# Optimization experiments

Measured on AMD Instinct MI355X. Metric: run time of the kernel, lower is better.

Reference implementation:

```python
import jax, jax.numpy as jnp
import numpy as np

T, B, D, H, L, O = 800, 32, 440, 1024, 4, 2000
EPS = 1e-5

def _bn(x, g, b, m, v):
    return (x - m) * jax.lax.rsqrt(v + EPS) * g + b

def setup_inputs() -> dict:
    key = jax.random.key(0)
    ks = jax.random.split(key, 12)
    s = 0.02
    return {
        "xs": jax.random.normal(ks[0], (T, B, D), dtype=jnp.float32),
        "w0": jax.random.normal(ks[1], (2 * H, D), dtype=jnp.float32) * s,
        "wr": jax.random.normal(ks[2], (L - 1, 2 * H, H), dtype=jnp.float32) * s,
        "bnz_g": jnp.ones((L, H), jnp.float32),
        "bnz_b": jnp.zeros((L, H), jnp.float32),
        "bnz_m": jax.random.normal(ks[3], (L, H), dtype=jnp.float32) * 0.1,
        "bnz_v": jax.random.uniform(ks[4], (L, H), dtype=jnp.float32) + 0.5,
        "bnc_g": jnp.ones((L, H), jnp.float32),
        "bnc_b": jnp.zeros((L, H), jnp.float32),
        "bnc_m": jax.random.normal(ks[5], (L, H), dtype=jnp.float32) * 0.1,
        "bnc_v": jax.random.uniform(ks[6], (L, H), dtype=jnp.float32) + 0.5,
        "wf": jax.random.normal(ks[7], (O, H), dtype=jnp.float32) * 0.003,
        "bnf_g": jnp.ones((O,), jnp.float32),
        "bnf_b": jnp.zeros((O,), jnp.float32),
        "bnf_m": jax.random.normal(ks[8], (O,), dtype=jnp.float32) * 0.1,
        "bnf_v": jax.random.uniform(ks[9], (O,), dtype=jnp.float32) + 0.5,
    }

def reference(xs, w0, wr, bnz_g, bnz_b, bnz_m, bnz_v, bnc_g, bnc_b, bnc_m, bnc_v, wf, bnf_g, bnf_b, bnf_m, bnf_v):
    x = xs  # [T,B,feat]
    for i in range(L):
        W = w0 if i == 0 else wr[i - 1]
        ws = jnp.einsum('tbd,hd->tbh', x, W)          # [T,B,2H]
        wz, wc = jnp.split(ws, 2, axis=-1)
        z = jax.nn.sigmoid(_bn(wz, bnz_g[i], bnz_b[i], bnz_m[i], bnz_v[i]))
        c = jax.nn.relu(_bn(wc, bnc_g[i], bnc_b[i], bnc_m[i], bnc_v[i]))
        def step(h, zc):
            z_t, c_t = zc
            h = (1.0 - z_t) * c_t + z_t * h
            return h, h
        _, hs = jax.lax.scan(step, jnp.zeros((B, H), x.dtype), (z, c))
        x = hs  # [T,B,H]
    out = jnp.einsum('tbh,oh->tbo', x, wf).reshape(T * B, O)
    out = _bn(out, bnf_g, bnf_b, bnf_m, bnf_v)
    return jax.nn.log_softmax(out, axis=1)
```

## Files before the change

### kernel.cpp

```cpp
#include <hip/hip_runtime.h>
#include <math.h>
#include <stdint.h>

#define T_ 800
#define B_ 32
#define D_ 440
#define DP_ 448
#define H_ 1024
#define L_ 4
#define O_ 2000
#define OP_ 2048
#define EPS_ 1e-5f
#define M_ (T_ * B_)
#define NC_ 8
#define TC_ (T_ / NC_)

#define BM 128
#define BN 128
#define BK 32

typedef __attribute__((ext_vector_type(8))) short bf16x8;
typedef __attribute__((ext_vector_type(4))) float f32x4;

__device__ inline float b2f(unsigned short u) {
    union { unsigned int i; float f; } v; v.i = ((unsigned int)u) << 16; return v.f;
}
__device__ inline unsigned short f2b(float f) {
    unsigned int x = __float_as_uint(f);
    return (unsigned short)((x + 0x7FFFu + ((x >> 16) & 1u)) >> 16);
}

__global__ void bn_prep(const float* __restrict__ g, const float* __restrict__ b,
                        const float* __restrict__ m, const float* __restrict__ v,
                        float* __restrict__ scale, float* __restrict__ bias,
                        int nsrc, int ndst)
{
    int i = blockIdx.x * 256 + threadIdx.x;
    if (i >= ndst) return;
    if (i < nsrc) {
        float s = g[i] * rsqrtf(v[i] + EPS_);
        scale[i] = s;
        bias[i] = fmaf(-m[i], s, b[i]);
    } else {
        scale[i] = 0.f;
        bias[i] = 0.f;
    }
}

__global__ void cvt_pad(const float* __restrict__ src, unsigned short* __restrict__ dst,
                        int Rs, int Cs, int Cd, int total)
{
    int i = blockIdx.x * 256 + threadIdx.x;
    if (i >= total) return;
    int r = i / Cd, c = i - r * Cd;
    float v = (r < Rs && c < Cs) ? src[(size_t)r * Cs + c] : 0.f;
    dst[i] = f2b(v);
}

__global__ __launch_bounds__(256) void gemm_bf16(
    const unsigned short* __restrict__ A, const unsigned short* __restrict__ Wt,
    int K, int mode,
    unsigned short* __restrict__ zout, unsigned short* __restrict__ cout,
    const float* __restrict__ zscale, const float* __restrict__ zbias,
    const float* __restrict__ cscale, const float* __restrict__ cbias,
    unsigned short* __restrict__ fout,
    const float* __restrict__ fscale, const float* __restrict__ fbias)
{
    __shared__ unsigned short As[BM * BK];
    __shared__ unsigned short Bs[BN * BK];

    const int tid = threadIdx.x;
    const int lane = tid & 63;
    const int wid = tid >> 6;
    const int wm = wid >> 1, wn = wid & 1;
    const int m0 = blockIdx.y * BM;
    const int n0 = blockIdx.x * BN;

    const int srow = lane >> 2;
    const int scol = (lane & 3) * 8;

    const int ca0 = wid * 2, ca1 = wid * 2 + 1;
    const unsigned short* aR0 = A + (size_t)(m0 + ca0 * 16 + srow) * K + scol;
    const unsigned short* aR1 = A + (size_t)(m0 + ca1 * 16 + srow) * K + scol;
    const int gn0 = n0 + ((ca0 >> 2) << 6) + srow * 4 + (ca0 & 3);
    const int gn1 = n0 + ((ca1 >> 2) << 6) + srow * 4 + (ca1 & 3);
    const unsigned short* bR0 = Wt + (size_t)gn0 * K + scol;
    const unsigned short* bR1 = Wt + (size_t)gn1 * K + scol;
    unsigned short* lA0 = As + ca0 * 16 * BK;
    unsigned short* lA1 = As + ca1 * 16 * BK;
    unsigned short* lB0 = Bs + ca0 * 16 * BK;
    unsigned short* lB1 = Bs + ca1 * 16 * BK;

    f32x4 acc[4][4];
    #pragma unroll
    for (int i = 0; i < 4; i++)
        #pragma unroll
        for (int j = 0; j < 4; j++)
            acc[i][j] = (f32x4){0.f, 0.f, 0.f, 0.f};

    const int fr = lane & 15;
    const int fk = (lane >> 4) * 8;

    for (int k0 = 0; k0 < K; k0 += BK) {
        __builtin_amdgcn_global_load_lds(
            (const __attribute__((address_space(1))) unsigned int*)(aR0 + k0),
            (__attribute__((address_space(3))) unsigned int*)lA0, 16, 0, 0);
        __builtin_amdgcn_global_load_lds(
            (const __attribute__((address_space(1))) unsigned int*)(aR1 + k0),
            (__attribute__((address_space(3))) unsigned int*)lA1, 16, 0, 0);
        __builtin_amdgcn_global_load_lds(
            (const __attribute__((address_space(1))) unsigned int*)(bR0 + k0),
            (__attribute__((address_space(3))) unsigned int*)lB0, 16, 0, 0);
        __builtin_amdgcn_global_load_lds(
            (const __attribute__((address_space(1))) unsigned int*)(bR1 + k0),
            (__attribute__((address_space(3))) unsigned int*)lB1, 16, 0, 0);
        __syncthreads();

        bf16x8 af[4], bfr[4];
        #pragma unroll
        for (int t = 0; t < 4; t++) {
            af[t]  = *(const bf16x8*)(As + (wm * 64 + t * 16 + fr) * BK + fk);
            bfr[t] = *(const bf16x8*)(Bs + (wn * 64 + t * 16 + fr) * BK + fk);
        }
        #pragma unroll
        for (int mi = 0; mi < 4; mi++)
            #pragma unroll
            for (int ni = 0; ni < 4; ni++)
                acc[mi][ni] = __builtin_amdgcn_mfma_f32_16x16x32_bf16(af[mi], bfr[ni], acc[mi][ni], 0, 0, 0);
        __syncthreads();
    }

    const int q = lane >> 4;
    const int colb = n0 + wn * 64 + (lane & 15) * 4;
    const int rbase = m0 + wm * 64 + q * 4;

    if (mode == 0) {
        const bool isz = (n0 < H_);
        const float* sc = isz ? zscale : cscale;
        const float* bi = isz ? zbias : cbias;
        unsigned short* dst = isz ? zout : cout;
        const int npb = isz ? colb : colb - H_;
        const float4 s4 = *(const float4*)(sc + npb);
        const float4 b4 = *(const float4*)(bi + npb);
        #pragma unroll
        for (int mi = 0; mi < 4; mi++)
            #pragma unroll
            for (int r = 0; r < 4; r++) {
                const int m = rbase + mi * 16 + r;
                float v0 = fmaf(acc[mi][0][r], s4.x, b4.x);
                float v1 = fmaf(acc[mi][1][r], s4.y, b4.y);
                float v2 = fmaf(acc[mi][2][r], s4.z, b4.z);
                float v3 = fmaf(acc[mi][3][r], s4.w, b4.w);
                if (isz) {
                    v0 = __builtin_amdgcn_rcpf(1.f + __expf(-v0));
                    v1 = __builtin_amdgcn_rcpf(1.f + __expf(-v1));
                    v2 = __builtin_amdgcn_rcpf(1.f + __expf(-v2));
                    v3 = __builtin_amdgcn_rcpf(1.f + __expf(-v3));
                } else {
                    v0 = fmaxf(v0, 0.f); v1 = fmaxf(v1, 0.f);
                    v2 = fmaxf(v2, 0.f); v3 = fmaxf(v3, 0.f);
                }
                ushort4 pk = make_ushort4(f2b(v0), f2b(v1), f2b(v2), f2b(v3));
                *(ushort4*)(dst + (size_t)m * H_ + npb) = pk;
            }
    } else {
        const float4 s4 = *(const float4*)(fscale + colb);
        const float4 b4 = *(const float4*)(fbias + colb);
        #pragma unroll
        for (int mi = 0; mi < 4; mi++)
            #pragma unroll
            for (int r = 0; r < 4; r++) {
                const int m = rbase + mi * 16 + r;
                ushort4 pk = make_ushort4(
                    f2b(fmaf(acc[mi][0][r], s4.x, b4.x)),
                    f2b(fmaf(acc[mi][1][r], s4.y, b4.y)),
                    f2b(fmaf(acc[mi][2][r], s4.z, b4.z)),
                    f2b(fmaf(acc[mi][3][r], s4.w, b4.w)));
                *(ushort4*)(fout + (size_t)m * OP_ + colb) = pk;
            }
    }
}

__global__ __launch_bounds__(256) void scan_pass1(
    const unsigned short* __restrict__ z, const unsigned short* __restrict__ c,
    float* __restrict__ H0, float* __restrict__ P)
{
    const int k = blockIdx.y;
    const int idx = blockIdx.x * 256 + threadIdx.x;
    float h = 0.f, p = 1.f;
    size_t off = (size_t)k * TC_ * (B_ * H_) + idx;
    #pragma unroll 4
    for (int t = 0; t < TC_; ++t) {
        float zt = b2f(z[off]);
        float ct = b2f(c[off]);
        h = fmaf(zt, h - ct, ct);
        p *= zt;
        off += (size_t)(B_ * H_);
    }
    H0[(size_t)k * (B_ * H_) + idx] = h;
    P[(size_t)k * (B_ * H_) + idx] = p;
}

__global__ __launch_bounds__(256) void scan_pass2(
    const unsigned short* __restrict__ z, const unsigned short* __restrict__ c,
    const float* __restrict__ H0, const float* __restrict__ P,
    unsigned short* __restrict__ x)
{
    const int k = blockIdx.y;
    const int idx = blockIdx.x * 256 + threadIdx.x;
    float h = 0.f;
    for (int j = 0; j < k; ++j)
        h = fmaf(P[(size_t)j * (B_ * H_) + idx], h, H0[(size_t)j * (B_ * H_) + idx]);
    size_t off = (size_t)k * TC_ * (B_ * H_) + idx;
    #pragma unroll 4
    for (int t = 0; t < TC_; ++t) {
        float zt = b2f(z[off]);
        float ct = b2f(c[off]);
        h = fmaf(zt, h - ct, ct);
        x[off] = f2b(h);
        off += (size_t)(B_ * H_);
    }
}

__global__ __launch_bounds__(256) void logsoftmax_kernel(
    const unsigned short* __restrict__ lg, float* __restrict__ out)
{
    const int row = blockIdx.x;
    const unsigned short* p = lg + (size_t)row * OP_;
    float* po = out + (size_t)row * O_;
    const int tid = threadIdx.x;

    float v[8];
    float mx = -1e30f;
    #pragma unroll
    for (int j = 0; j < 8; j++) {
        int col = tid + j * 256;
        v[j] = (col < O_) ? b2f(p[col]) : -1e30f;
        mx = fmaxf(mx, v[j]);
    }
    #pragma unroll
    for (int o = 32; o > 0; o >>= 1) mx = fmaxf(mx, __shfl_down(mx, o));
    __shared__ float smax[4];
    __shared__ float ssum[4];
    const int lane = tid & 63, wid = tid >> 6;
    if (lane == 0) smax[wid] = mx;
    __syncthreads();
    mx = fmaxf(fmaxf(smax[0], smax[1]), fmaxf(smax[2], smax[3]));

    float s = 0.f;
    #pragma unroll
    for (int j = 0; j < 8; j++) {
        int col = tid + j * 256;
        if (col < O_) s += expf(v[j] - mx);
    }
    #pragma unroll
    for (int o = 32; o > 0; o >>= 1) s += __shfl_down(s, o);
    if (lane == 0) ssum[wid] = s;
    __syncthreads();
    s = ssum[0] + ssum[1] + ssum[2] + ssum[3];
    const float lse = mx + logf(s);

    #pragma unroll
    for (int j = 0; j < 8; j++) {
        int col = tid + j * 256;
        if (col < O_) po[col] = v[j] - lse;
    }
}

extern "C" void kernel_launch(void* const* d_in, const int* in_sizes, int n_in,
                              void* d_out, int out_size, void* d_ws, size_t ws_size,
                              hipStream_t stream)
{
    (void)in_sizes; (void)n_in; (void)out_size; (void)ws_size;

    const float* xs    = (const float*)d_in[0];
    const float* w0    = (const float*)d_in[1];
    const float* wr    = (const float*)d_in[2];
    const float* bnz_g = (const float*)d_in[3];
    const float* bnz_b = (const float*)d_in[4];
    const float* bnz_m = (const float*)d_in[5];
    const float* bnz_v = (const float*)d_in[6];
    const float* bnc_g = (const float*)d_in[7];
    const float* bnc_b = (const float*)d_in[8];
    const float* bnc_m = (const float*)d_in[9];
    const float* bnc_v = (const float*)d_in[10];
    const float* wf    = (const float*)d_in[11];
    const float* bnf_g = (const float*)d_in[12];
    const float* bnf_b = (const float*)d_in[13];
    const float* bnf_m = (const float*)d_in[14];
    const float* bnf_v = (const float*)d_in[15];
    float* out = (float*)d_out;

    unsigned short* p = (unsigned short*)d_ws;
    unsigned short* xbuf  = p;  p += (size_t)M_ * H_;
    unsigned short* x0buf = p;  p += (size_t)M_ * DP_;
    unsigned short* zbuf  = p;  p += (size_t)M_ * H_;
    unsigned short* cbuf  = p;  p += (size_t)M_ * H_;
    unsigned short* w0p   = p;  p += (size_t)(2 * H_) * DP_;
    unsigned short* wrp   = p;  p += (size_t)(L_ - 1) * (2 * H_) * H_;
    unsigned short* wfp   = p;  p += (size_t)OP_ * H_;
    unsigned short* lbuf  = p;  p += (size_t)M_ * OP_;
    float* fp = (float*)p;
    float* zs = fp;  fp += L_ * H_;
    float* zb = fp;  fp += L_ * H_;
    float* cs = fp;  fp += L_ * H_;
    float* cb = fp;  fp += L_ * H_;
    float* fs = fp;  fp += OP_;
    float* fb = fp;  fp += OP_;
    float* sH0 = fp; fp += NC_ * B_ * H_;
    float* sP  = fp;

    dim3 blk(256);
    bn_prep<<<(L_ * H_ + 255) / 256, blk, 0, stream>>>(bnz_g, bnz_b, bnz_m, bnz_v, zs, zb, L_ * H_, L_ * H_);
    bn_prep<<<(L_ * H_ + 255) / 256, blk, 0, stream>>>(bnc_g, bnc_b, bnc_m, bnc_v, cs, cb, L_ * H_, L_ * H_);
    bn_prep<<<(OP_ + 255) / 256, blk, 0, stream>>>(bnf_g, bnf_b, bnf_m, bnf_v, fs, fb, O_, OP_);

    {
        int t0 = M_ * DP_;
        cvt_pad<<<(t0 + 255) / 256, blk, 0, stream>>>(xs, x0buf, M_, D_, DP_, t0);
        int t1 = 2 * H_ * DP_;
        cvt_pad<<<(t1 + 255) / 256, blk, 0, stream>>>(w0, w0p, 2 * H_, D_, DP_, t1);
        int t2 = (L_ - 1) * 2 * H_ * H_;
        cvt_pad<<<(t2 + 255) / 256, blk, 0, stream>>>(wr, wrp, (L_ - 1) * 2 * H_, H_, H_, t2);
        int t3 = OP_ * H_;
        cvt_pad<<<(t3 + 255) / 256, blk, 0, stream>>>(wf, wfp, O_, H_, H_, t3);
    }

    dim3 sgrid((B_ * H_) / 256, NC_);
    for (int layer = 0; layer < L_; ++layer) {
        const unsigned short* Ain = (layer == 0) ? x0buf : xbuf;
        const unsigned short* W   = (layer == 0) ? w0p : (wrp + (size_t)(layer - 1) * (2 * H_) * H_);
        const int K               = (layer == 0) ? DP_ : H_;
        dim3 grid((2 * H_) / BN, M_ / BM);
        gemm_bf16<<<grid, blk, 0, stream>>>(Ain, W, K, 0,
            zbuf, cbuf,
            zs + layer * H_, zb + layer * H_, cs + layer * H_, cb + layer * H_,
            nullptr, nullptr, nullptr);
        scan_pass1<<<sgrid, blk, 0, stream>>>(zbuf, cbuf, sH0, sP);
        scan_pass2<<<sgrid, blk, 0, stream>>>(zbuf, cbuf, sH0, sP, xbuf);
    }

    dim3 gridf(OP_ / BN, M_ / BM);
    gemm_bf16<<<gridf, blk, 0, stream>>>(xbuf, wfp, H_, 1,
        nullptr, nullptr, nullptr, nullptr, nullptr, nullptr,
        lbuf, fs, fb);

    logsoftmax_kernel<<<M_, blk, 0, stream>>>(lbuf, out);
}
```

Baseline: 1.328 ms.

## Double-buffer GEMM LDS tiles, vectorize scan and conversion kernels, more scan chunks

```diff
diff --git a/kernel.cpp b/kernel.cpp
--- a/kernel.cpp
+++ b/kernel.cpp
@@ -12,7 +12,8 @@
 #define OP_ 2048
 #define EPS_ 1e-5f
 #define M_ (T_ * B_)
-#define NC_ 8
+#define BH_ (B_ * H_)
+#define NC_ 16
 #define TC_ (T_ / NC_)
 
 #define BM 128
@@ -47,14 +48,26 @@
     }
 }
 
-__global__ void cvt_pad(const float* __restrict__ src, unsigned short* __restrict__ dst,
-                        int Rs, int Cs, int Cd, int total)
+__global__ void cvt_pad8(const float* __restrict__ src, unsigned short* __restrict__ dst,
+                         int Rs, int Cs, int Cd, int total8)
 {
     int i = blockIdx.x * 256 + threadIdx.x;
-    if (i >= total) return;
-    int r = i / Cd, c = i - r * Cd;
-    float v = (r < Rs && c < Cs) ? src[(size_t)r * Cs + c] : 0.f;
-    dst[i] = f2b(v);
+    if (i >= total8) return;
+    const int c8 = Cd >> 3;
+    int r = i / c8, c = (i - r * c8) << 3;
+    ushort4 lo, hi;
+    if (r < Rs && c < Cs) {
+        const float4 a = *(const float4*)(src + (size_t)r * Cs + c);
+        const float4 b = *(const float4*)(src + (size_t)r * Cs + c + 4);
+        lo = make_ushort4(f2b(a.x), f2b(a.y), f2b(a.z), f2b(a.w));
+        hi = make_ushort4(f2b(b.x), f2b(b.y), f2b(b.z), f2b(b.w));
+    } else {
+        lo = make_ushort4(0, 0, 0, 0);
+        hi = make_ushort4(0, 0, 0, 0);
+    }
+    unsigned short* d = dst + (size_t)r * Cd + c;
+    *(ushort4*)d = lo;
+    *(ushort4*)(d + 4) = hi;
 }
 
 __global__ __launch_bounds__(256) void gemm_bf16(
@@ -66,8 +79,8 @@
     unsigned short* __restrict__ fout,
     const float* __restrict__ fscale, const float* __restrict__ fbias)
 {
-    __shared__ unsigned short As[BM * BK];
-    __shared__ unsigned short Bs[BN * BK];
+    __shared__ unsigned short As[2][BM * BK];
+    __shared__ unsigned short Bs[2][BN * BK];
 
     const int tid = threadIdx.x;
     const int lane = tid & 63;
@@ -86,10 +99,8 @@
     const int gn1 = n0 + ((ca1 >> 2) << 6) + srow * 4 + (ca1 & 3);
     const unsigned short* bR0 = Wt + (size_t)gn0 * K + scol;
     const unsigned short* bR1 = Wt + (size_t)gn1 * K + scol;
-    unsigned short* lA0 = As + ca0 * 16 * BK;
-    unsigned short* lA1 = As + ca1 * 16 * BK;
-    unsigned short* lB0 = Bs + ca0 * 16 * BK;
-    unsigned short* lB1 = Bs + ca1 * 16 * BK;
+    const int lofsA0 = ca0 * 16 * BK;
+    const int lofsA1 = ca1 * 16 * BK;
 
     f32x4 acc[4][4];
     #pragma unroll
@@ -101,33 +112,56 @@
     const int fr = lane & 15;
     const int fk = (lane >> 4) * 8;
 
-    for (int k0 = 0; k0 < K; k0 += BK) {
+    const int nIters = K / BK;
+
+    {
         __builtin_amdgcn_global_load_lds(
-            (const __attribute__((address_space(1))) unsigned int*)(aR0 + k0),
-            (__attribute__((address_space(3))) unsigned int*)lA0, 16, 0, 0);
+            (const __attribute__((address_space(1))) unsigned int*)aR0,
+            (__attribute__((address_space(3))) unsigned int*)(As[0] + lofsA0), 16, 0, 0);
         __builtin_amdgcn_global_load_lds(
-            (const __attribute__((address_space(1))) unsigned int*)(aR1 + k0),
-            (__attribute__((address_space(3))) unsigned int*)lA1, 16, 0, 0);
+            (const __attribute__((address_space(1))) unsigned int*)aR1,
+            (__attribute__((address_space(3))) unsigned int*)(As[0] + lofsA1), 16, 0, 0);
         __builtin_amdgcn_global_load_lds(
-            (const __attribute__((address_space(1))) unsigned int*)(bR0 + k0),
-            (__attribute__((address_space(3))) unsigned int*)lB0, 16, 0, 0);
+            (const __attribute__((address_space(1))) unsigned int*)bR0,
+            (__attribute__((address_space(3))) unsigned int*)(Bs[0] + lofsA0), 16, 0, 0);
         __builtin_amdgcn_global_load_lds(
-            (const __attribute__((address_space(1))) unsigned int*)(bR1 + k0),
-            (__attribute__((address_space(3))) unsigned int*)lB1, 16, 0, 0);
+            (const __attribute__((address_space(1))) unsigned int*)bR1,
+            (__attribute__((address_space(3))) unsigned int*)(Bs[0] + lofsA1), 16, 0, 0);
+    }
+
+    for (int it = 0; it < nIters; ++it) {
         __syncthreads();
 
+        if (it + 1 < nIters) {
+            const int nk = (it + 1) * BK;
+            const int nb = (it + 1) & 1;
+            __builtin_amdgcn_global_load_lds(
+                (const __attribute__((address_space(1))) unsigned int*)(aR0 + nk),
+                (__attribute__((address_space(3))) unsigned int*)(As[nb] + lofsA0), 16, 0, 0);
+            __builtin_amdgcn_global_load_lds(
+                (const __attribute__((address_space(1))) unsigned int*)(aR1 + nk),
+                (__attribute__((address_space(3))) unsigned int*)(As[nb] + lofsA1), 16, 0, 0);
+            __builtin_amdgcn_global_load_lds(
+                (const __attribute__((address_space(1))) unsigned int*)(bR0 + nk),
+                (__attribute__((address_space(3))) unsigned int*)(Bs[nb] + lofsA0), 16, 0, 0);
+            __builtin_amdgcn_global_load_lds(
+                (const __attribute__((address_space(1))) unsigned int*)(bR1 + nk),
+                (__attribute__((address_space(3))) unsigned int*)(Bs[nb] + lofsA1), 16, 0, 0);
+        }
+
+        const unsigned short* curA = As[it & 1];
+        const unsigned short* curB = Bs[it & 1];
         bf16x8 af[4], bfr[4];
         #pragma unroll
         for (int t = 0; t < 4; t++) {
-            af[t]  = *(const bf16x8*)(As + (wm * 64 + t * 16 + fr) * BK + fk);
-            bfr[t] = *(const bf16x8*)(Bs + (wn * 64 + t * 16 + fr) * BK + fk);
+            af[t]  = *(const bf16x8*)(curA + (wm * 64 + t * 16 + fr) * BK + fk);
+            bfr[t] = *(const bf16x8*)(curB + (wn * 64 + t * 16 + fr) * BK + fk);
         }
         #pragma unroll
         for (int mi = 0; mi < 4; mi++)
             #pragma unroll
             for (int ni = 0; ni < 4; ni++)
                 acc[mi][ni] = __builtin_amdgcn_mfma_f32_16x16x32_bf16(af[mi], bfr[ni], acc[mi][ni], 0, 0, 0);
-        __syncthreads();
     }
 
     const int q = lane >> 4;
@@ -186,19 +220,22 @@
     float* __restrict__ H0, float* __restrict__ P)
 {
     const int k = blockIdx.y;
-    const int idx = blockIdx.x * 256 + threadIdx.x;
-    float h = 0.f, p = 1.f;
-    size_t off = (size_t)k * TC_ * (B_ * H_) + idx;
-    #pragma unroll 4
+    const int e2 = blockIdx.x * 256 + threadIdx.x;
+    float h0 = 0.f, h1 = 0.f, p0 = 1.f, p1 = 1.f;
+    size_t off = ((size_t)k * TC_ * BH_ + 2 * e2) >> 1;
+    const unsigned int* z32 = (const unsigned int*)z;
+    const unsigned int* c32 = (const unsigned int*)c;
+    #pragma unroll 5
     for (int t = 0; t < TC_; ++t) {
-        float zt = b2f(z[off]);
-        float ct = b2f(c[off]);
-        h = fmaf(zt, h - ct, ct);
-        p *= zt;
-        off += (size_t)(B_ * H_);
-    }
-    H0[(size_t)k * (B_ * H_) + idx] = h;
-    P[(size_t)k * (B_ * H_) + idx] = p;
+        unsigned int zz = z32[off], cc = c32[off];
+        float z0 = b2f((unsigned short)zz), z1 = b2f((unsigned short)(zz >> 16));
+        float c0 = b2f((unsigned short)cc), c1 = b2f((unsigned short)(cc >> 16));
+        h0 = fmaf(z0, h0 - c0, c0);  p0 *= z0;
+        h1 = fmaf(z1, h1 - c1, c1);  p1 *= z1;
+        off += BH_ / 2;
+    }
+    *(float2*)(H0 + (size_t)k * BH_ + 2 * e2) = make_float2(h0, h1);
+    *(float2*)(P  + (size_t)k * BH_ + 2 * e2) = make_float2(p0, p1);
 }
 
 __global__ __launch_bounds__(256) void scan_pass2(
@@ -207,18 +244,27 @@
     unsigned short* __restrict__ x)
 {
     const int k = blockIdx.y;
-    const int idx = blockIdx.x * 256 + threadIdx.x;
-    float h = 0.f;
-    for (int j = 0; j < k; ++j)
-        h = fmaf(P[(size_t)j * (B_ * H_) + idx], h, H0[(size_t)j * (B_ * H_) + idx]);
-    size_t off = (size_t)k * TC_ * (B_ * H_) + idx;
-    #pragma unroll 4
+    const int e2 = blockIdx.x * 256 + threadIdx.x;
+    float h0 = 0.f, h1 = 0.f;
+    for (int j = 0; j < k; ++j) {
+        float2 pj = *(const float2*)(P  + (size_t)j * BH_ + 2 * e2);
+        float2 hj = *(const float2*)(H0 + (size_t)j * BH_ + 2 * e2);
+        h0 = fmaf(pj.x, h0, hj.x);
+        h1 = fmaf(pj.y, h1, hj.y);
+    }
+    size_t off = ((size_t)k * TC_ * BH_ + 2 * e2) >> 1;
+    const unsigned int* z32 = (const unsigned int*)z;
+    const unsigned int* c32 = (const unsigned int*)c;
+    unsigned int* x32 = (unsigned int*)x;
+    #pragma unroll 5
     for (int t = 0; t < TC_; ++t) {
-        float zt = b2f(z[off]);
-        float ct = b2f(c[off]);
-        h = fmaf(zt, h - ct, ct);
-        x[off] = f2b(h);
-        off += (size_t)(B_ * H_);
+        unsigned int zz = z32[off], cc = c32[off];
+        float z0 = b2f((unsigned short)zz), z1 = b2f((unsigned short)(zz >> 16));
+        float c0 = b2f((unsigned short)cc), c1 = b2f((unsigned short)(cc >> 16));
+        h0 = fmaf(z0, h0 - c0, c0);
+        h1 = fmaf(z1, h1 - c1, c1);
+        x32[off] = (unsigned int)f2b(h0) | ((unsigned int)f2b(h1) << 16);
+        off += BH_ / 2;
     }
 }
 
@@ -307,7 +353,7 @@
     float* cb = fp;  fp += L_ * H_;
     float* fs = fp;  fp += OP_;
     float* fb = fp;  fp += OP_;
-    float* sH0 = fp; fp += NC_ * B_ * H_;
+    float* sH0 = fp; fp += NC_ * BH_;
     float* sP  = fp;
 
     dim3 blk(256);
@@ -316,17 +362,18 @@
     bn_prep<<<(OP_ + 255) / 256, blk, 0, stream>>>(bnf_g, bnf_b, bnf_m, bnf_v, fs, fb, O_, OP_);
 
     {
-        int t0 = M_ * DP_;
-        cvt_pad<<<(t0 + 255) / 256, blk, 0, stream>>>(xs, x0buf, M_, D_, DP_, t0);
-        int t1 = 2 * H_ * DP_;
-        cvt_pad<<<(t1 + 255) / 256, blk, 0, stream>>>(w0, w0p, 2 * H_, D_, DP_, t1);
-        int t2 = (L_ - 1) * 2 * H_ * H_;
-        cvt_pad<<<(t2 + 255) / 256, blk, 0, stream>>>(wr, wrp, (L_ - 1) * 2 * H_, H_, H_, t2);
-        int t3 = OP_ * H_;
-        cvt_pad<<<(t3 + 255) / 256, blk, 0, stream>>>(wf, wfp, O_, H_, H_, t3);
-    }
-
-    dim3 sgrid((B_ * H_) / 256, NC_);
+        int t0 = M_ * DP_ / 8;
+        cvt_pad8<<<(t0 + 255) / 256, blk, 0, stream>>>(xs, x0buf, M_, D_, DP_, t0);
+        int t1 = 2 * H_ * DP_ / 8;
+        cvt_pad8<<<(t1 + 255) / 256, blk, 0, stream>>>(w0, w0p, 2 * H_, D_, DP_, t1);
+        int t2 = (L_ - 1) * 2 * H_ * H_ / 8;
+        cvt_pad8<<<(t2 + 255) / 256, blk, 0, stream>>>(wr, wrp, (L_ - 1) * 2 * H_, H_, H_, t2);
+        int t3 = OP_ * H_ / 8;
+        cvt_pad8<<<(t3 + 255) / 256, blk, 0, stream>>>(wf, wfp, O_, H_, H_, t3);
+    }
+
+    dim3 sgrid1(BH_ / 512, NC_ - 1);
+    dim3 sgrid2(BH_ / 512, NC_);
     for (int layer = 0; layer < L_; ++layer) {
         const unsigned short* Ain = (layer == 0) ? x0buf : xbuf;
         const unsigned short* W   = (layer == 0) ? w0p : (wrp + (size_t)(layer - 1) * (2 * H_) * H_);
@@ -336,8 +383,8 @@
             zbuf, cbuf,
             zs + layer * H_, zb + layer * H_, cs + layer * H_, cb + layer * H_,
             nullptr, nullptr, nullptr);
-        scan_pass1<<<sgrid, blk, 0, stream>>>(zbuf, cbuf, sH0, sP);
-        scan_pass2<<<sgrid, blk, 0, stream>>>(zbuf, cbuf, sH0, sP, xbuf);
+        scan_pass1<<<sgrid1, blk, 0, stream>>>(zbuf, cbuf, sH0, sP);
+        scan_pass2<<<sgrid2, blk, 0, stream>>>(zbuf, cbuf, sH0, sP, xbuf);
     }
 
     dim3 gridf(OP_ / BN, M_ / BM);
```

Measured after the change: 1.238 ms. 6.8% less time.
